# Kernel optimization log

Measured on AMD Instinct MI355X. Metric: run time of the kernel, lower is better.

Reference implementation:

```python
import jax, jax.numpy as jnp
import numpy as np

B, S, E, H = 4, 2048, 768, 12
D = E // H  # head dimension = 64


def setup_inputs() -> dict:
    key = jax.random.key(0)
    ks = jax.random.split(key, 10)
    scale = 1.0 / np.sqrt(E)
    x = jax.random.normal(ks[0], (B, S, E), dtype=jnp.float32)
    mask = jax.random.randint(ks[1], (B, S), 0, 2, dtype=jnp.int32)
    # per-head Q/K/V projections stacked over heads: [H, E, D]
    Wq = jax.random.normal(ks[2], (H, E, D), dtype=jnp.float32) * scale
    bq = jax.random.normal(ks[3], (H, D), dtype=jnp.float32) * scale
    Wk = jax.random.normal(ks[4], (H, E, D), dtype=jnp.float32) * scale
    bk = jax.random.normal(ks[5], (H, D), dtype=jnp.float32) * scale
    Wv = jax.random.normal(ks[6], (H, E, D), dtype=jnp.float32) * scale
    bv = jax.random.normal(ks[7], (H, D), dtype=jnp.float32) * scale
    # output projection: [H*D, E]
    Wo = jax.random.normal(ks[8], (H * D, E), dtype=jnp.float32) * scale
    bo = jax.random.normal(ks[9], (E,), dtype=jnp.float32) * scale
    return {"x": x, "mask": mask, "Wq": Wq, "bq": bq, "Wk": Wk, "bk": bk,
            "Wv": Wv, "bv": bv, "Wo": Wo, "bo": bo}


def reference(x, mask, Wq, bq, Wk, bk, Wv, bv, Wo, bo):
    # Per-head linear projections, vectorized over heads: [B, H, S, D]
    q = jnp.einsum('bse,hed->bhsd', x, Wq) + bq[None, :, None, :]
    k = jnp.einsum('bse,hed->bhsd', x, Wk) + bk[None, :, None, :]
    v = jnp.einsum('bse,hed->bhsd', x, Wv) + bv[None, :, None, :]
    # scores: [B, H, S, S]
    scores = jnp.einsum('bhqd,bhkd->bhqk', q, k) / jnp.sqrt(jnp.float32(D))
    # mask [B, S] broadcast over heads and query positions (key-side mask)
    key_mask = mask[:, None, None, :]  # [B, 1, 1, S]
    scores = jnp.where(key_mask == 0, jnp.float32(-1e9), scores)
    attn = jax.nn.softmax(scores, axis=-1)
    out = jnp.einsum('bhqk,bhkd->bhqd', attn, v)  # [B, H, S, D]
    # concat heads: [B, S, H*D]
    out = out.transpose(0, 2, 1, 3).reshape(B, S, H * D)
    return out @ Wo + bo
```

## Files before the change

### kernel.cpp

```cpp
#include <hip/hip_runtime.h>
#include <hip/hip_bf16.h>

#define B_ 4
#define S_ 2048
#define E_ 768
#define H_ 12
#define D_ 64
#define M_ (B_*S_)
#define NQKV 2304
#define KDIM 768

typedef __bf16 bf16x8 __attribute__((ext_vector_type(8)));
typedef float f32x4 __attribute__((ext_vector_type(4)));
typedef short shortx4 __attribute__((ext_vector_type(4)));
typedef unsigned int uintx2 __attribute__((ext_vector_type(2)));
typedef unsigned int uintx4 __attribute__((ext_vector_type(4)));

typedef __attribute__((address_space(1))) void gvoid;
typedef __attribute__((address_space(3))) void lvoid;

__device__ __forceinline__ void gl_lds16(const void* g, void* l) {
  __builtin_amdgcn_global_load_lds((gvoid*)g, (lvoid*)l, 16, 0, 0);
}

__device__ __forceinline__ f32x4 mfma16(bf16x8 a, bf16x8 b, f32x4 c) {
  return __builtin_amdgcn_mfma_f32_16x16x32_bf16(a, b, c, 0, 0, 0);
}

__device__ __forceinline__ f32x4 mfma_pv(shortx4 a, shortx4 b, f32x4 c) {
#if __has_builtin(__builtin_amdgcn_mfma_f32_16x16x16bf16_1k)
  return __builtin_amdgcn_mfma_f32_16x16x16bf16_1k(a, b, c, 0, 0, 0);
#else
  uintx2 au = __builtin_bit_cast(uintx2, a);
  uintx2 bu = __builtin_bit_cast(uintx2, b);
  uintx4 aw = {au.x, au.y, 0u, 0u};
  uintx4 bw = {bu.x, bu.y, 0u, 0u};
  return mfma16(__builtin_bit_cast(bf16x8, aw), __builtin_bit_cast(bf16x8, bw), c);
#endif
}

__device__ __forceinline__ __bf16 ldmix(const void* p, size_t idx, int is_bf) {
  if (is_bf) return ((const __bf16*)p)[idx];
  return (__bf16)(((const float*)p)[idx]);
}
__device__ __forceinline__ float ldmixf(const void* p, size_t idx, int is_bf) {
  if (is_bf) return (float)((const __bf16*)p)[idx];
  return ((const float*)p)[idx];
}

__global__ void detect_kernel(const unsigned short* __restrict__ xr, int* __restrict__ flag) {
  __shared__ int cnt;
  if (threadIdx.x == 0) cnt = 0;
  __syncthreads();
  unsigned short h = xr[2 * threadIdx.x];
  int e = (h >> 7) & 0xFF;
  if (e >= 100 && e <= 140) atomicAdd(&cnt, 1);
  __syncthreads();
  if (threadIdx.x == 0) *flag = (cnt > 148) ? 1 : 0;
}

__global__ __launch_bounds__(256) void convx_kernel(const void* __restrict__ x,
                                                    const int* __restrict__ flag,
                                                    __bf16* __restrict__ Xb) {
  const int is_bf = *flag;
  int idx = blockIdx.x * 256 + threadIdx.x;
  Xb[idx] = ldmix(x, idx, is_bf);
}

__global__ __launch_bounds__(256) void scan_kernel(
    const int* __restrict__ mask,
    int* __restrict__ R,
    float* __restrict__ maskC,
    int* __restrict__ npadArr)
{
  __shared__ int wtot[4];
  __shared__ int runningS;
  const int t = threadIdx.x;
  const int w = t >> 6, lane = t & 63;
  const int b = blockIdx.x;
  if (t == 0) runningS = 0;
  __syncthreads();
  for (int k0 = 0; k0 < S_; k0 += 256) {
    int keep = (mask[b * S_ + k0 + t] != 0) ? 1 : 0;
    unsigned long long bal = __ballot(keep);
    int lanePre = __popcll(bal & ((1ull << lane) - 1ull));
    if (lane == 0) wtot[w] = __popcll(bal);
    __syncthreads();
    int base = runningS;
    for (int i = 0; i < w; ++i) base += wtot[i];
    if (keep) {
      int pos = base + lanePre;
      R[b * S_ + pos] = b * S_ + k0 + t;
      maskC[b * S_ + pos] = 0.f;
    }
    __syncthreads();
    if (t == 0) runningS += wtot[0] + wtot[1] + wtot[2] + wtot[3];
    __syncthreads();
  }
  int n = runningS;
  int np = (n + 63) & ~63;
  for (int j = n + t; j < S_; j += 256) {
    R[b * S_ + j] = b * S_;
    maskC[b * S_ + j] = -1.0e9f;
  }
  if (t == 0) npadArr[b] = np;
}

__global__ __launch_bounds__(256) void pack_kernel(
    const void* __restrict__ Wq, const void* __restrict__ bq,
    const void* __restrict__ Wk, const void* __restrict__ bk,
    const void* __restrict__ Wv, const void* __restrict__ bv,
    const void* __restrict__ Wo, const void* __restrict__ bo,
    const int* __restrict__ flag,
    __bf16* __restrict__ WbT, __bf16* __restrict__ WoT,
    float* __restrict__ biasP, float* __restrict__ biasO)
{
  const int is_bf = *flag;
  int idx = blockIdx.x * 256 + threadIdx.x;
  const int NW = NQKV * KDIM;
  if (idx < NW) {
    int n = idx / KDIM;
    int e = idx - n * KDIM;
    int sel = n / 768;
    int hd  = n - sel * 768;
    int h = hd >> 6, d = hd & 63;
    const void* W = (sel == 0) ? Wq : (sel == 1) ? Wk : Wv;
    WbT[idx] = ldmix(W, (size_t)(h * 768 + e) * 64 + d, is_bf);
  } else {
    int idx2 = idx - NW;
    int n = idx2 / 768;
    int k = idx2 - n * 768;
    WoT[idx2] = ldmix(Wo, (size_t)k * 768 + n, is_bf);
  }
  if (idx < NQKV) {
    int sel = idx / 768;
    int hd = idx - sel * 768;
    const void* bsel = (sel == 0) ? bq : (sel == 1) ? bk : bv;
    biasP[idx] = ldmixf(bsel, hd, is_bf);
  }
  if (idx >= NW && idx < NW + 768) {
    biasO[idx - NW] = ldmixf(bo, idx - NW, is_bf);
  }
}

__global__ __launch_bounds__(256) void gemm_bt_bias(
    const __bf16* __restrict__ A,
    const __bf16* __restrict__ Bt,
    const float* __restrict__ bias,
    void* __restrict__ C,
    int N, int K,
    const int* __restrict__ flag, int force_bf16)
{
  __shared__ __align__(16) __bf16 As[128 * 32];
  __shared__ __align__(16) __bf16 Bs[128 * 32];
  const int obf = force_bf16 | *flag;
  const int t = threadIdx.x;
  const int wave = t >> 6, lane = t & 63;
  const int l15 = lane & 15, lq = lane >> 4;
  const int m0 = blockIdx.x * 128;
  const int n0 = blockIdx.y * 128;
  const int wr = (wave >> 1) * 64;
  const int wc = (wave & 1) * 64;

  const f32x4 z4 = {0.f, 0.f, 0.f, 0.f};
  f32x4 acc[4][4];
  for (int i = 0; i < 4; ++i)
    for (int j = 0; j < 4; ++j) acc[i][j] = z4;

  for (int k0 = 0; k0 < K; k0 += 32) {
    __syncthreads();
    for (int p = 0; p < 2; ++p) {
      int chunk = p * 256 + t;
      int row = chunk >> 2, c8 = (chunk & 3) << 3;
      gl_lds16(A  + (size_t)(m0 + row) * K + k0 + c8, As + (size_t)(p * 256 + wave * 64) * 8);
      gl_lds16(Bt + (size_t)(n0 + row) * K + k0 + c8, Bs + (size_t)(p * 256 + wave * 64) * 8);
    }
    __syncthreads();
    bf16x8 af[4], bfr[4];
    for (int i = 0; i < 4; ++i) af[i]  = *(const bf16x8*)(As + (wr + i * 16 + l15) * 32 + lq * 8);
    for (int j = 0; j < 4; ++j) bfr[j] = *(const bf16x8*)(Bs + (wc + j * 16 + l15) * 32 + lq * 8);
    for (int i = 0; i < 4; ++i)
      for (int j = 0; j < 4; ++j)
        acc[i][j] = mfma16(af[i], bfr[j], acc[i][j]);
  }

  for (int j = 0; j < 4; ++j) {
    int n = n0 + wc + j * 16 + l15;
    float bv = bias[n];
    for (int i = 0; i < 4; ++i) {
      int mbase = m0 + wr + i * 16 + lq * 4;
      for (int r = 0; r < 4; ++r) {
        size_t off = (size_t)(mbase + r) * N + n;
        float val = acc[i][j][r] + bv;
        if (obf) ((__bf16*)C)[off] = (__bf16)val;
        else     ((float*)C)[off]  = val;
      }
    }
  }
}

__global__ __launch_bounds__(256) void gemm_kv(
    const __bf16* __restrict__ Xb,
    const __bf16* __restrict__ WbT,
    const float* __restrict__ biasP,
    const int* __restrict__ R,
    const int* __restrict__ npadArr,
    __bf16* __restrict__ Kc,
    __bf16* __restrict__ Vc)
{
  __shared__ __align__(16) __bf16 As[128 * 32];
  __shared__ __align__(16) __bf16 Bs[128 * 32];
  const int t = threadIdx.x;
  const int wave = t >> 6, lane = t & 63;
  const int l15 = lane & 15, lq = lane >> 4;
  const int b = blockIdx.z;
  const int j0 = blockIdx.x * 128;
  if (j0 >= npadArr[b]) return;
  const int n0 = blockIdx.y * 128;
  const int wr = (wave >> 1) * 64;
  const int wc = (wave & 1) * 64;
  const int c8 = (t & 3) << 3;

  const int rowA0 = R[b * S_ + j0 + ((0 * 256 + t) >> 2)];
  const int rowA1 = R[b * S_ + j0 + ((1 * 256 + t) >> 2)];

  const f32x4 z4 = {0.f, 0.f, 0.f, 0.f};
  f32x4 acc[4][4];
  for (int i = 0; i < 4; ++i)
    for (int j = 0; j < 4; ++j) acc[i][j] = z4;

  for (int k0 = 0; k0 < KDIM; k0 += 32) {
    __syncthreads();
    gl_lds16(Xb + (size_t)rowA0 * KDIM + k0 + c8, As + (size_t)(0 * 256 + wave * 64) * 8);
    gl_lds16(Xb + (size_t)rowA1 * KDIM + k0 + c8, As + (size_t)(1 * 256 + wave * 64) * 8);
    for (int p = 0; p < 2; ++p) {
      int chunk = p * 256 + t;
      int row = chunk >> 2;
      gl_lds16(WbT + (size_t)(768 + n0 + row) * KDIM + k0 + c8, Bs + (size_t)(p * 256 + wave * 64) * 8);
    }
    __syncthreads();
    bf16x8 af[4], bfr[4];
    for (int i = 0; i < 4; ++i) af[i]  = *(const bf16x8*)(As + (wr + i * 16 + l15) * 32 + lq * 8);
    for (int j = 0; j < 4; ++j) bfr[j] = *(const bf16x8*)(Bs + (wc + j * 16 + l15) * 32 + lq * 8);
    for (int i = 0; i < 4; ++i)
      for (int j = 0; j < 4; ++j)
        acc[i][j] = mfma16(af[i], bfr[j], acc[i][j]);
  }

  for (int j = 0; j < 4; ++j) {
    int n = n0 + wc + j * 16 + l15;
    float bv = biasP[768 + n];
    const int isK = (n < 768);
    const int hh = (isK ? n : n - 768) >> 6;
    const int d  = n & 63;
    const size_t bhh = (size_t)(b * H_ + hh);
    for (int i = 0; i < 4; ++i) {
      int jbase = j0 + wr + i * 16 + lq * 4;
      for (int r = 0; r < 4; ++r) {
        int jj = jbase + r;
        __bf16 ov = (__bf16)(acc[i][j][r] + bv);
        if (isK) Kc[(bhh * 2048 + jj) * 64 + d] = ov;
        else     Vc[(bhh * 512 + (jj >> 2)) * 256 + d * 4 + (jj & 3)] = ov;
      }
    }
  }
}

__global__ __launch_bounds__(256) void attn_kernel(
    const __bf16* __restrict__ Qc,
    const __bf16* __restrict__ Kc,
    const __bf16* __restrict__ Vc,
    const float* __restrict__ maskC,
    const int* __restrict__ npadArr,
    __bf16* __restrict__ Out)
{
  __shared__ __align__(16) __bf16 Ks0[64 * 32];
  __shared__ __align__(16) __bf16 Ks1[64 * 32];
  __shared__ __align__(16) __bf16 Vt[16 * 256];
  __shared__ __align__(16) float msk[64];

  const int t = threadIdx.x;
  const int w = t >> 6, lane = t & 63;
  const int l15 = lane & 15, qd = lane >> 4;
  const int bh = blockIdx.y;
  const int b = bh / H_, h = bh - b * H_;
  const int q0 = blockIdx.x * 128;
  const int Skv = npadArr[b];

  const __bf16* Qb = Qc + (size_t)b * S_ * E_ + h * 64;
  const __bf16* Kb = Kc + (size_t)bh * 2048 * 64;
  const __bf16* Vg = Vc + (size_t)bh * 512 * 256;
  const float* mb = maskC + b * S_;

  bf16x8 qf[2][2];
#pragma unroll
  for (int sub = 0; sub < 2; ++sub) {
    int qrow = q0 + w * 32 + sub * 16 + l15;
    qf[sub][0] = *(const bf16x8*)(Qb + (size_t)qrow * E_ + qd * 8);
    qf[sub][1] = *(const bf16x8*)(Qb + (size_t)qrow * E_ + 32 + qd * 8);
  }

  const f32x4 z4 = {0.f, 0.f, 0.f, 0.f};
  f32x4 o[2][4];
#pragma unroll
  for (int sub = 0; sub < 2; ++sub)
#pragma unroll
    for (int dt = 0; dt < 4; ++dt) o[sub][dt] = z4;
  f32x4 ol[2] = {z4, z4};

  const short one_bf = (short)0x3F80;
  const shortx4 ones4 = {one_bf, one_bf, one_bf, one_bf};

  const int skey = t >> 2;
  const int sch  = (t & 3) * 8;
  const float SC = 0.18033688011112042f;

  for (int k0 = 0; k0 < Skv; k0 += 64) {
    __syncthreads();
    gl_lds16(Kb + (size_t)(k0 + skey) * 64 + sch,      Ks0 + w * 512);
    gl_lds16(Kb + (size_t)(k0 + skey) * 64 + 32 + sch, Ks1 + w * 512);
    {
      const __bf16* vsrc = Vg + ((size_t)(k0 >> 2)) * 256;
      gl_lds16(vsrc + t * 8,        Vt + w * 512);
      gl_lds16(vsrc + 2048 + t * 8, Vt + 2048 + w * 512);
    }
    if (t < 16) gl_lds16(mb + k0 + lane * 4, msk);
    __syncthreads();

    bf16x8 kf[4][2];
#pragma unroll
    for (int kt = 0; kt < 4; ++kt) {
      kf[kt][0] = *(const bf16x8*)(Ks0 + (kt * 16 + l15) * 32 + qd * 8);
      kf[kt][1] = *(const bf16x8*)(Ks1 + (kt * 16 + l15) * 32 + qd * 8);
    }
    shortx4 vf[4][4];
#pragma unroll
    for (int kt = 0; kt < 4; ++kt)
#pragma unroll
      for (int dt = 0; dt < 4; ++dt)
        vf[kt][dt] = *(const shortx4*)(Vt + (kt * 4 + qd) * 256 + (dt * 16 + l15) * 4);
    f32x4 ma[4];
#pragma unroll
    for (int kt = 0; kt < 4; ++kt) ma[kt] = *(const f32x4*)(msk + kt * 16 + qd * 4);

#pragma unroll
    for (int sub = 0; sub < 2; ++sub) {
      f32x4 s[4];
#pragma unroll
      for (int kt = 0; kt < 4; ++kt) {
        s[kt] = mfma16(kf[kt][0], qf[sub][0], z4);
        s[kt] = mfma16(kf[kt][1], qf[sub][1], s[kt]);
      }
      shortx4 pfr[4];
#pragma unroll
      for (int kt = 0; kt < 4; ++kt) {
        float p0 = __builtin_amdgcn_exp2f(__builtin_fmaf(s[kt][0], SC, ma[kt][0]));
        float p1 = __builtin_amdgcn_exp2f(__builtin_fmaf(s[kt][1], SC, ma[kt][1]));
        float p2 = __builtin_amdgcn_exp2f(__builtin_fmaf(s[kt][2], SC, ma[kt][2]));
        float p3 = __builtin_amdgcn_exp2f(__builtin_fmaf(s[kt][3], SC, ma[kt][3]));
        unsigned int lo16 = __builtin_amdgcn_perm(__builtin_bit_cast(unsigned int, p1),
                                                  __builtin_bit_cast(unsigned int, p0), 0x07060302u);
        unsigned int hi16 = __builtin_amdgcn_perm(__builtin_bit_cast(unsigned int, p3),
                                                  __builtin_bit_cast(unsigned int, p2), 0x07060302u);
        uintx2 u = {lo16, hi16};
        pfr[kt] = __builtin_bit_cast(shortx4, u);
      }
#pragma unroll
      for (int dt = 0; dt < 4; ++dt)
#pragma unroll
        for (int kt = 0; kt < 4; ++kt)
          o[sub][dt] = mfma_pv(pfr[kt], vf[kt][dt], o[sub][dt]);
#pragma unroll
      for (int kt = 0; kt < 4; ++kt)
        ol[sub] = mfma_pv(pfr[kt], ones4, ol[sub]);
    }
  }

#pragma unroll
  for (int sub = 0; sub < 2; ++sub) {
#pragma unroll
    for (int dt = 0; dt < 4; ++dt)
#pragma unroll
      for (int r = 0; r < 4; ++r) {
        int qrow = q0 + w * 32 + sub * 16 + qd * 4 + r;
        Out[(size_t)(b * S_ + qrow) * E_ + h * 64 + dt * 16 + l15] =
            (__bf16)(o[sub][dt][r] / ol[sub][r]);
      }
  }
}

extern "C" void kernel_launch(void* const* d_in, const int* in_sizes, int n_in,
                              void* d_out, int out_size, void* d_ws, size_t ws_size,
                              hipStream_t stream) {
  const void* x  = d_in[0];
  const int* mask = (const int*)d_in[1];
  const void* Wq = d_in[2];
  const void* bq = d_in[3];
  const void* Wk = d_in[4];
  const void* bk = d_in[5];
  const void* Wv = d_in[6];
  const void* bv = d_in[7];
  const void* Wo = d_in[8];
  const void* bo = d_in[9];

  char* ws = (char*)d_ws;
  int*    flag  = (int*)(ws + 0);
  __bf16* Xb    = (__bf16*)(ws + 256);
  __bf16* WbT   = (__bf16*)(ws + 12583168);
  __bf16* WoT   = (__bf16*)(ws + 16122112);
  float*  biasP = (float*)(ws + 17301760);
  float*  biasO = (float*)(ws + 17310976);
  __bf16* Qc    = (__bf16*)(ws + 17314048);
  __bf16* Kc    = (__bf16*)(ws + 29896960);
  __bf16* Vc    = (__bf16*)(ws + 42479872);
  __bf16* attnO = (__bf16*)(ws + 55062784);
  int*    Ridx  = (int*)(ws + 67645696);
  float*  maskC = (float*)(ws + 67678464);
  int*    npad  = (int*)(ws + 67711232);

  detect_kernel<<<dim3(1), dim3(256), 0, stream>>>((const unsigned short*)x, flag);
  convx_kernel<<<dim3(24576), dim3(256), 0, stream>>>(x, flag, Xb);
  scan_kernel<<<dim3(B_), dim3(256), 0, stream>>>(mask, Ridx, maskC, npad);
  pack_kernel<<<dim3(9216), dim3(256), 0, stream>>>(Wq, bq, Wk, bk, Wv, bv, Wo, bo, flag,
                                                    WbT, WoT, biasP, biasO);
  gemm_bt_bias<<<dim3(64, 6), dim3(256), 0, stream>>>(Xb, WbT, biasP, Qc, E_, KDIM, flag, 1);
  gemm_kv<<<dim3(16, 12, B_), dim3(256), 0, stream>>>(Xb, WbT, biasP, Ridx, npad, Kc, Vc);
  attn_kernel<<<dim3(16, 48), dim3(256), 0, stream>>>(Qc, Kc, Vc, maskC, npad, attnO);
  gemm_bt_bias<<<dim3(64, 6), dim3(256), 0, stream>>>(attnO, WoT, biasO, d_out, E_, KDIM, flag, 0);
}
```

Baseline: 242.5 us.

## Merge prep kernels, fuse Q and KV projections, shrink GEMM tiles

Folds detect and mask scan into one launch, and folds the x conversion into the weight-pack kernel with 8-wide vectorized loads. Q and K/V projections become a single gemm_qkv launch over a flat grid. Both GEMMs drop from 128x128 to 128x64 tiles so more blocks fill the CUs. The aim is fewer kernel launches and better occupancy and load balance, at the cost of less operand reuse per tile.

```diff
diff --git a/kernel.cpp b/kernel.cpp
--- a/kernel.cpp
+++ b/kernel.cpp
@@ -48,36 +48,27 @@
   return ((const float*)p)[idx];
 }
 
-__global__ void detect_kernel(const unsigned short* __restrict__ xr, int* __restrict__ flag) {
+__global__ __launch_bounds__(256) void detect_scan_kernel(
+    const unsigned short* __restrict__ xr, int* __restrict__ flag,
+    const int* __restrict__ mask,
+    int* __restrict__ R, float* __restrict__ maskC, int* __restrict__ npadArr)
+{
   __shared__ int cnt;
-  if (threadIdx.x == 0) cnt = 0;
-  __syncthreads();
-  unsigned short h = xr[2 * threadIdx.x];
-  int e = (h >> 7) & 0xFF;
-  if (e >= 100 && e <= 140) atomicAdd(&cnt, 1);
-  __syncthreads();
-  if (threadIdx.x == 0) *flag = (cnt > 148) ? 1 : 0;
-}
-
-__global__ __launch_bounds__(256) void convx_kernel(const void* __restrict__ x,
-                                                    const int* __restrict__ flag,
-                                                    __bf16* __restrict__ Xb) {
-  const int is_bf = *flag;
-  int idx = blockIdx.x * 256 + threadIdx.x;
-  Xb[idx] = ldmix(x, idx, is_bf);
-}
-
-__global__ __launch_bounds__(256) void scan_kernel(
-    const int* __restrict__ mask,
-    int* __restrict__ R,
-    float* __restrict__ maskC,
-    int* __restrict__ npadArr)
-{
   __shared__ int wtot[4];
   __shared__ int runningS;
   const int t = threadIdx.x;
+  if (blockIdx.x == 0) {
+    if (t == 0) cnt = 0;
+    __syncthreads();
+    unsigned short h = xr[2 * t];
+    int e = (h >> 7) & 0xFF;
+    if (e >= 100 && e <= 140) atomicAdd(&cnt, 1);
+    __syncthreads();
+    if (t == 0) *flag = (cnt > 148) ? 1 : 0;
+    return;
+  }
   const int w = t >> 6, lane = t & 63;
-  const int b = blockIdx.x;
+  const int b = blockIdx.x - 1;
   if (t == 0) runningS = 0;
   __syncthreads();
   for (int k0 = 0; k0 < S_; k0 += 256) {
@@ -106,17 +97,35 @@
   if (t == 0) npadArr[b] = np;
 }
 
-__global__ __launch_bounds__(256) void pack_kernel(
+__global__ __launch_bounds__(256) void prep_kernel(
+    const void* __restrict__ x,
     const void* __restrict__ Wq, const void* __restrict__ bq,
     const void* __restrict__ Wk, const void* __restrict__ bk,
     const void* __restrict__ Wv, const void* __restrict__ bv,
     const void* __restrict__ Wo, const void* __restrict__ bo,
     const int* __restrict__ flag,
+    __bf16* __restrict__ Xb,
     __bf16* __restrict__ WbT, __bf16* __restrict__ WoT,
     float* __restrict__ biasP, float* __restrict__ biasO)
 {
   const int is_bf = *flag;
-  int idx = blockIdx.x * 256 + threadIdx.x;
+  const int bid = blockIdx.x;
+  const int t = threadIdx.x;
+  if (bid < 3072) {
+    int base = (bid * 256 + t) * 8;
+    if (is_bf) {
+      *(uintx4*)(Xb + base) = *(const uintx4*)((const __bf16*)x + base);
+    } else {
+      const float* xf = (const float*)x + base;
+      f32x4 a = *(const f32x4*)xf;
+      f32x4 c = *(const f32x4*)(xf + 4);
+      __bf16 ov[8] = {(__bf16)a[0], (__bf16)a[1], (__bf16)a[2], (__bf16)a[3],
+                      (__bf16)c[0], (__bf16)c[1], (__bf16)c[2], (__bf16)c[3]};
+      *(uintx4*)(Xb + base) = *(uintx4*)ov;
+    }
+    return;
+  }
+  int idx = (bid - 3072) * 256 + t;
   const int NW = NQKV * KDIM;
   if (idx < NW) {
     int n = idx / KDIM;
@@ -143,124 +152,165 @@
   }
 }
 
-__global__ __launch_bounds__(256) void gemm_bt_bias(
-    const __bf16* __restrict__ A,
-    const __bf16* __restrict__ Bt,
-    const float* __restrict__ bias,
-    void* __restrict__ C,
-    int N, int K,
-    const int* __restrict__ flag, int force_bf16)
-{
-  __shared__ __align__(16) __bf16 As[128 * 32];
-  __shared__ __align__(16) __bf16 Bs[128 * 32];
-  const int obf = force_bf16 | *flag;
-  const int t = threadIdx.x;
-  const int wave = t >> 6, lane = t & 63;
-  const int l15 = lane & 15, lq = lane >> 4;
-  const int m0 = blockIdx.x * 128;
-  const int n0 = blockIdx.y * 128;
-  const int wr = (wave >> 1) * 64;
-  const int wc = (wave & 1) * 64;
-
-  const f32x4 z4 = {0.f, 0.f, 0.f, 0.f};
-  f32x4 acc[4][4];
-  for (int i = 0; i < 4; ++i)
-    for (int j = 0; j < 4; ++j) acc[i][j] = z4;
-
-  for (int k0 = 0; k0 < K; k0 += 32) {
-    __syncthreads();
-    for (int p = 0; p < 2; ++p) {
-      int chunk = p * 256 + t;
-      int row = chunk >> 2, c8 = (chunk & 3) << 3;
-      gl_lds16(A  + (size_t)(m0 + row) * K + k0 + c8, As + (size_t)(p * 256 + wave * 64) * 8);
-      gl_lds16(Bt + (size_t)(n0 + row) * K + k0 + c8, Bs + (size_t)(p * 256 + wave * 64) * 8);
-    }
-    __syncthreads();
-    bf16x8 af[4], bfr[4];
-    for (int i = 0; i < 4; ++i) af[i]  = *(const bf16x8*)(As + (wr + i * 16 + l15) * 32 + lq * 8);
-    for (int j = 0; j < 4; ++j) bfr[j] = *(const bf16x8*)(Bs + (wc + j * 16 + l15) * 32 + lq * 8);
-    for (int i = 0; i < 4; ++i)
-      for (int j = 0; j < 4; ++j)
-        acc[i][j] = mfma16(af[i], bfr[j], acc[i][j]);
-  }
-
-  for (int j = 0; j < 4; ++j) {
-    int n = n0 + wc + j * 16 + l15;
-    float bv = bias[n];
-    for (int i = 0; i < 4; ++i) {
-      int mbase = m0 + wr + i * 16 + lq * 4;
-      for (int r = 0; r < 4; ++r) {
-        size_t off = (size_t)(mbase + r) * N + n;
-        float val = acc[i][j][r] + bv;
-        if (obf) ((__bf16*)C)[off] = (__bf16)val;
-        else     ((float*)C)[off]  = val;
-      }
-    }
-  }
-}
-
-__global__ __launch_bounds__(256) void gemm_kv(
+__global__ __launch_bounds__(256) void gemm_qkv(
     const __bf16* __restrict__ Xb,
     const __bf16* __restrict__ WbT,
     const float* __restrict__ biasP,
     const int* __restrict__ R,
     const int* __restrict__ npadArr,
+    __bf16* __restrict__ Qc,
     __bf16* __restrict__ Kc,
     __bf16* __restrict__ Vc)
 {
   __shared__ __align__(16) __bf16 As[128 * 32];
-  __shared__ __align__(16) __bf16 Bs[128 * 32];
+  __shared__ __align__(16) __bf16 Bs[64 * 32];
   const int t = threadIdx.x;
   const int wave = t >> 6, lane = t & 63;
   const int l15 = lane & 15, lq = lane >> 4;
-  const int b = blockIdx.z;
-  const int j0 = blockIdx.x * 128;
-  if (j0 >= npadArr[b]) return;
-  const int n0 = blockIdx.y * 128;
-  const int wr = (wave >> 1) * 64;
-  const int wc = (wave & 1) * 64;
+  const int wm = (wave & 1) * 64;
+  const int wn = (wave >> 1) * 32;
+
+  const int bid = blockIdx.x;
+  int m0, bn0, isQ, b = 0;
+  int rowA0, rowA1;
+  if (bid < 768) {
+    isQ = 1;
+    int mi = bid / 12, ni = bid - mi * 12;
+    m0 = mi * 128; bn0 = ni * 64;
+    rowA0 = m0 + ((0 * 256 + t) >> 2);
+    rowA1 = m0 + ((1 * 256 + t) >> 2);
+  } else {
+    isQ = 0;
+    int r2 = bid - 768;
+    b = r2 / 384;
+    int rr = r2 - b * 384;
+    int mi = rr / 24, ni = rr - mi * 24;
+    if (mi * 128 >= npadArr[b]) return;
+    m0 = mi * 128;
+    bn0 = 768 + ni * 64;
+    rowA0 = R[b * S_ + m0 + ((0 * 256 + t) >> 2)];
+    rowA1 = R[b * S_ + m0 + ((1 * 256 + t) >> 2)];
+  }
   const int c8 = (t & 3) << 3;
-
-  const int rowA0 = R[b * S_ + j0 + ((0 * 256 + t) >> 2)];
-  const int rowA1 = R[b * S_ + j0 + ((1 * 256 + t) >> 2)];
+  const int brow = t >> 2;
 
   const f32x4 z4 = {0.f, 0.f, 0.f, 0.f};
-  f32x4 acc[4][4];
+  f32x4 acc[4][2];
+#pragma unroll
   for (int i = 0; i < 4; ++i)
-    for (int j = 0; j < 4; ++j) acc[i][j] = z4;
+#pragma unroll
+    for (int j = 0; j < 2; ++j) acc[i][j] = z4;
 
   for (int k0 = 0; k0 < KDIM; k0 += 32) {
     __syncthreads();
-    gl_lds16(Xb + (size_t)rowA0 * KDIM + k0 + c8, As + (size_t)(0 * 256 + wave * 64) * 8);
-    gl_lds16(Xb + (size_t)rowA1 * KDIM + k0 + c8, As + (size_t)(1 * 256 + wave * 64) * 8);
-    for (int p = 0; p < 2; ++p) {
-      int chunk = p * 256 + t;
-      int row = chunk >> 2;
-      gl_lds16(WbT + (size_t)(768 + n0 + row) * KDIM + k0 + c8, Bs + (size_t)(p * 256 + wave * 64) * 8);
-    }
-    __syncthreads();
-    bf16x8 af[4], bfr[4];
-    for (int i = 0; i < 4; ++i) af[i]  = *(const bf16x8*)(As + (wr + i * 16 + l15) * 32 + lq * 8);
-    for (int j = 0; j < 4; ++j) bfr[j] = *(const bf16x8*)(Bs + (wc + j * 16 + l15) * 32 + lq * 8);
+    gl_lds16(Xb + (size_t)rowA0 * KDIM + k0 + c8, As + (size_t)(wave * 64) * 8);
+    gl_lds16(Xb + (size_t)rowA1 * KDIM + k0 + c8, As + (size_t)(256 + wave * 64) * 8);
+    gl_lds16(WbT + (size_t)(bn0 + brow) * KDIM + k0 + c8, Bs + (size_t)(wave * 64) * 8);
+    __syncthreads();
+    bf16x8 af[4], bfr[2];
+#pragma unroll
+    for (int i = 0; i < 4; ++i) af[i]  = *(const bf16x8*)(As + (wm + i * 16 + l15) * 32 + lq * 8);
+#pragma unroll
+    for (int j = 0; j < 2; ++j) bfr[j] = *(const bf16x8*)(Bs + (wn + j * 16 + l15) * 32 + lq * 8);
+#pragma unroll
     for (int i = 0; i < 4; ++i)
-      for (int j = 0; j < 4; ++j)
+#pragma unroll
+      for (int j = 0; j < 2; ++j)
         acc[i][j] = mfma16(af[i], bfr[j], acc[i][j]);
   }
 
-  for (int j = 0; j < 4; ++j) {
-    int n = n0 + wc + j * 16 + l15;
-    float bv = biasP[768 + n];
-    const int isK = (n < 768);
-    const int hh = (isK ? n : n - 768) >> 6;
-    const int d  = n & 63;
-    const size_t bhh = (size_t)(b * H_ + hh);
+#pragma unroll
+  for (int j = 0; j < 2; ++j) {
+    int nn = (bn0 - (isQ ? 0 : 768)) + wn + j * 16 + l15;
+    float bv = biasP[(isQ ? 0 : 768) + nn];
+    if (isQ) {
+#pragma unroll
+      for (int i = 0; i < 4; ++i) {
+        int mbase = m0 + wm + i * 16 + lq * 4;
+#pragma unroll
+        for (int r = 0; r < 4; ++r)
+          Qc[(size_t)(mbase + r) * 768 + nn] = (__bf16)(acc[i][j][r] + bv);
+      }
+    } else {
+      const int isK = (nn < 768);
+      const int hh = (isK ? nn : nn - 768) >> 6;
+      const int d  = nn & 63;
+      const size_t bhh = (size_t)(b * H_ + hh);
+#pragma unroll
+      for (int i = 0; i < 4; ++i) {
+        int jbase = m0 + wm + i * 16 + lq * 4;
+#pragma unroll
+        for (int r = 0; r < 4; ++r) {
+          int jj = jbase + r;
+          __bf16 ov = (__bf16)(acc[i][j][r] + bv);
+          if (isK) Kc[(bhh * 2048 + jj) * 64 + d] = ov;
+          else     Vc[(bhh * 512 + (jj >> 2)) * 256 + d * 4 + (jj & 3)] = ov;
+        }
+      }
+    }
+  }
+}
+
+__global__ __launch_bounds__(256) void gemm_out(
+    const __bf16* __restrict__ A,
+    const __bf16* __restrict__ WoT,
+    const float* __restrict__ biasO,
+    void* __restrict__ C,
+    const int* __restrict__ flag)
+{
+  __shared__ __align__(16) __bf16 As[128 * 32];
+  __shared__ __align__(16) __bf16 Bs[64 * 32];
+  const int obf = *flag;
+  const int t = threadIdx.x;
+  const int wave = t >> 6, lane = t & 63;
+  const int l15 = lane & 15, lq = lane >> 4;
+  const int wm = (wave & 1) * 64;
+  const int wn = (wave >> 1) * 32;
+  const int m0 = blockIdx.x * 128;
+  const int n0 = blockIdx.y * 64;
+  const int c8 = (t & 3) << 3;
+  const int brow = t >> 2;
+  const int rowA0 = m0 + ((0 * 256 + t) >> 2);
+  const int rowA1 = m0 + ((1 * 256 + t) >> 2);
+
+  const f32x4 z4 = {0.f, 0.f, 0.f, 0.f};
+  f32x4 acc[4][2];
+#pragma unroll
+  for (int i = 0; i < 4; ++i)
+#pragma unroll
+    for (int j = 0; j < 2; ++j) acc[i][j] = z4;
+
+  for (int k0 = 0; k0 < KDIM; k0 += 32) {
+    __syncthreads();
+    gl_lds16(A + (size_t)rowA0 * KDIM + k0 + c8, As + (size_t)(wave * 64) * 8);
+    gl_lds16(A + (size_t)rowA1 * KDIM + k0 + c8, As + (size_t)(256 + wave * 64) * 8);
+    gl_lds16(WoT + (size_t)(n0 + brow) * KDIM + k0 + c8, Bs + (size_t)(wave * 64) * 8);
+    __syncthreads();
+    bf16x8 af[4], bfr[2];
+#pragma unroll
+    for (int i = 0; i < 4; ++i) af[i]  = *(const bf16x8*)(As + (wm + i * 16 + l15) * 32 + lq * 8);
+#pragma unroll
+    for (int j = 0; j < 2; ++j) bfr[j] = *(const bf16x8*)(Bs + (wn + j * 16 + l15) * 32 + lq * 8);
+#pragma unroll
+    for (int i = 0; i < 4; ++i)
+#pragma unroll
+      for (int j = 0; j < 2; ++j)
+        acc[i][j] = mfma16(af[i], bfr[j], acc[i][j]);
+  }
+
+#pragma unroll
+  for (int j = 0; j < 2; ++j) {
+    int n = n0 + wn + j * 16 + l15;
+    float bv = biasO[n];
+#pragma unroll
     for (int i = 0; i < 4; ++i) {
-      int jbase = j0 + wr + i * 16 + lq * 4;
+      int mbase = m0 + wm + i * 16 + lq * 4;
+#pragma unroll
       for (int r = 0; r < 4; ++r) {
-        int jj = jbase + r;
-        __bf16 ov = (__bf16)(acc[i][j][r] + bv);
-        if (isK) Kc[(bhh * 2048 + jj) * 64 + d] = ov;
-        else     Vc[(bhh * 512 + (jj >> 2)) * 256 + d * 4 + (jj & 3)] = ov;
+        size_t off = (size_t)(mbase + r) * 768 + n;
+        float val = acc[i][j][r] + bv;
+        if (obf) ((__bf16*)C)[off] = (__bf16)val;
+        else     ((float*)C)[off]  = val;
       }
     }
   }
@@ -418,13 +468,11 @@
   float*  maskC = (float*)(ws + 67678464);
   int*    npad  = (int*)(ws + 67711232);
 
-  detect_kernel<<<dim3(1), dim3(256), 0, stream>>>((const unsigned short*)x, flag);
-  convx_kernel<<<dim3(24576), dim3(256), 0, stream>>>(x, flag, Xb);
-  scan_kernel<<<dim3(B_), dim3(256), 0, stream>>>(mask, Ridx, maskC, npad);
-  pack_kernel<<<dim3(9216), dim3(256), 0, stream>>>(Wq, bq, Wk, bk, Wv, bv, Wo, bo, flag,
-                                                    WbT, WoT, biasP, biasO);
-  gemm_bt_bias<<<dim3(64, 6), dim3(256), 0, stream>>>(Xb, WbT, biasP, Qc, E_, KDIM, flag, 1);
-  gemm_kv<<<dim3(16, 12, B_), dim3(256), 0, stream>>>(Xb, WbT, biasP, Ridx, npad, Kc, Vc);
+  detect_scan_kernel<<<dim3(5), dim3(256), 0, stream>>>(
+      (const unsigned short*)x, flag, mask, Ridx, maskC, npad);
+  prep_kernel<<<dim3(12288), dim3(256), 0, stream>>>(
+      x, Wq, bq, Wk, bk, Wv, bv, Wo, bo, flag, Xb, WbT, WoT, biasP, biasO);
+  gemm_qkv<<<dim3(2304), dim3(256), 0, stream>>>(Xb, WbT, biasP, Ridx, npad, Qc, Kc, Vc);
   attn_kernel<<<dim3(16, 48), dim3(256), 0, stream>>>(Qc, Kc, Vc, maskC, npad, attnO);
-  gemm_bt_bias<<<dim3(64, 6), dim3(256), 0, stream>>>(attnO, WoT, biasO, d_out, E_, KDIM, flag, 0);
-}
+  gemm_out<<<dim3(64, 12), dim3(256), 0, stream>>>(attnO, WoT, biasO, d_out, flag);
+}
```

Measured after the change: 221.8 us. -8.6%, faster.
